# Performance work log

Measured on AMD Instinct MI355X. Metric: run time of the kernel, lower is better.

The kernel has to match this reference:

```python
import jax, jax.numpy as jnp
import numpy as np

EMB = 256
HEADS = 8
DEPTH = EMB // HEADS
IN_CH = 256
ROW_LEN, COL_LEN = 50, 100
H, W = 50, 100


def setup_inputs() -> dict:
    key = jax.random.key(0)
    ks = jax.random.split(key, 16)
    d2 = EMB // 2
    return {
        "x": jax.random.normal(ks[0], (IN_CH, H, W), jnp.float32),
        "context": jax.random.normal(ks[1], (IN_CH, H, W), jnp.float32),
        "pad_mask": jax.random.randint(ks[2], (1, H * W, H * W), 0, 2) == 1,
        # learned 2D positional embeddings (uniform init, as in reset_parameters)
        "row_embed": jax.random.uniform(ks[3], (ROW_LEN, d2), jnp.float32),
        "col_embed": jax.random.uniform(ks[4], (COL_LEN, d2), jnp.float32),
        # proj_in: Conv2d(in_ch, emb, 1) -> weight [emb, in_ch], bias [emb]
        "w_in": jax.random.normal(ks[5], (EMB, IN_CH), jnp.float32) / np.sqrt(IN_CH),
        "b_in": jax.random.normal(ks[6], (EMB,), jnp.float32) * 0.01,
        "wq": jax.random.normal(ks[7], (EMB, EMB), jnp.float32) / np.sqrt(EMB),
        "bq": jax.random.normal(ks[8], (EMB,), jnp.float32) * 0.01,
        "wk": jax.random.normal(ks[9], (EMB, EMB), jnp.float32) / np.sqrt(EMB),
        "bk": jax.random.normal(ks[10], (EMB,), jnp.float32) * 0.01,
        "wv": jax.random.normal(ks[11], (EMB, EMB), jnp.float32) / np.sqrt(EMB),
        "bv": jax.random.normal(ks[12], (EMB,), jnp.float32) * 0.01,
        # proj_out: Conv2d(emb, in_ch, 1) -> weight [in_ch, emb], bias [in_ch]
        "w_out": jax.random.normal(ks[13], (IN_CH, EMB), jnp.float32) / np.sqrt(EMB),
        "b_out": jax.random.normal(ks[14], (IN_CH,), jnp.float32) * 0.01,
    }


def _pos_encoding(h, w, row_embed, col_embed):
    # returns [emb, h, w]: first half column embeds, second half row embeds
    d2 = row_embed.shape[1]
    xe = jnp.broadcast_to(col_embed[:w][None, :, :], (h, w, d2))  # (h,w,d2)
    ye = jnp.broadcast_to(row_embed[:h][:, None, :], (h, w, d2))  # (h,w,d2)
    return jnp.concatenate([xe, ye], axis=-1).transpose(2, 0, 1)


def _embed_tokens(img, pos, w_in, b_in):
    # img: [c,h,w] -> tokens [1, h*w, emb]
    y = img + pos                                   # [c,h,w]
    y = jnp.einsum('chw,ec->ehw', y, w_in) + b_in[:, None, None]
    e, h, w = y.shape
    return y.reshape(e, h * w).T[None]              # [1, hw, e]


def reference(x, context, pad_mask, row_embed, col_embed, w_in, b_in,
              wq, bq, wk, bk, wv, bv, w_out, b_out):
    c, h, w = x.shape
    pos = _pos_encoding(h, w, row_embed, col_embed)
    xt = _embed_tokens(x, pos, w_in, b_in)          # [1, N, e]
    ct = _embed_tokens(context, pos, w_in, b_in)    # [1, N, e]

    q = xt @ wq.T + bq
    k = ct @ wk.T + bk
    v = ct @ wv.T + bv
    b, n, _ = q.shape
    q = q.reshape(b, n, HEADS, DEPTH).transpose(0, 2, 1, 3)  # [1,H,N,d]
    k = k.reshape(b, n, HEADS, DEPTH).transpose(0, 2, 1, 3)
    v = v.reshape(b, n, HEADS, DEPTH).transpose(0, 2, 1, 3)

    scale = EMB ** (-0.5)  # note: module scales by emb_dim, not depth
    att = jnp.einsum('bnid,bnjd->bnij', q, k) * scale
    att = jnp.where(pad_mask[:, None, :, :], jnp.float32(-1e9), att)
    att = jax.nn.softmax(att, axis=-1)
    out = jnp.einsum('bnij,bnjd->bnid', att, v)     # [1,H,N,d]

    out = out.transpose(0, 2, 1, 3).reshape(b, n, EMB)       # [1,N,e]
    out = out[0].T.reshape(EMB, h, w)                        # [e,h,w]
    out = jnp.einsum('ehw,ce->chw', out, w_out) + b_out[:, None, None]
    return out
```

## Files before the change

### kernel.cpp

```cpp
#include <hip/hip_runtime.h>
#include <hip/hip_bf16.h>
#include <math.h>

#define N_TOK 5000
#define EMB_D 256
#define W_DIM 100
#define TPAD 5120
#define QPAD 5056
#define NKT  157
#define NKT_PAD 160
#define NSPLIT 8
#define TILES_PS 20
#define NB_EMBED (2 * NKT)
#define NB_MASKQ 20

typedef __attribute__((ext_vector_type(8)))  short short8_t;
typedef __attribute__((ext_vector_type(16))) float f32x16;
typedef __attribute__((ext_vector_type(2)))  unsigned uint2v;

__device__ __forceinline__ unsigned f2bf(float x) {
    union { float f; unsigned u; } c; c.f = x;
    return (c.u + 0x8000u) >> 16;
}
__device__ __forceinline__ unsigned pack2bf(float lo, float hi) {
    __hip_bfloat162 h2 = __float22bfloat162_rn(make_float2(lo, hi));
    union { __hip_bfloat162 h; unsigned u; } c; c.h = h2;
    return c.u;
}
__device__ __forceinline__ short8_t mkfrag(const f32x16& c, int cb) {
    const int b = 8 * cb;
    unsigned a0 = pack2bf(c[b + 0], c[b + 1]);
    unsigned a1 = pack2bf(c[b + 2], c[b + 3]);
    unsigned b0 = pack2bf(c[b + 4], c[b + 5]);
    unsigned b1 = pack2bf(c[b + 6], c[b + 7]);
    uint2v s02 = __builtin_amdgcn_permlane32_swap(a0, b0, false, false);
    uint2v s13 = __builtin_amdgcn_permlane32_swap(a1, b1, false, false);
    union { unsigned u[4]; short8_t v; } fr;
    fr.u[0] = s02.x; fr.u[1] = s13.x; fr.u[2] = s02.y; fr.u[3] = s13.y;
    return fr.v;
}

__global__ __launch_bounds__(256) void wb16_kernel(
    const float* __restrict__ w_in, const float* __restrict__ wq,
    const float* __restrict__ wk, const float* __restrict__ wv,
    const float* __restrict__ w_out, unsigned short* __restrict__ Wb)
{
    const float* srcs[5] = {w_in, wq, wk, wv, w_out};
    const float* s = srcs[blockIdx.y];
    unsigned short* d = Wb + (size_t)blockIdx.y * 65536;
    int i = (blockIdx.x * 256 + threadIdx.x) * 4;
    float4 v = *(const float4*)(s + i);
    uint2 u;
    u.x = pack2bf(v.x, v.y);
    u.y = pack2bf(v.z, v.w);
    *(uint2*)&d[i] = u;
}

__device__ __forceinline__ void gemm2_rowmajor(
    const short8_t* tokfr, const unsigned short* __restrict__ W,
    const float* __restrict__ bias, float sc,
    unsigned short* __restrict__ dst, int tok, int l31, int h, int w)
{
    const int chb = 8 * h;
    #pragma unroll
    for (int i = 0; i < 2; ++i) {
        const int ot = 2 * w + i;
        f32x16 c;
        #pragma unroll
        for (int r = 0; r < 16; ++r) c[r] = 0.f;
        #pragma unroll
        for (int blk = 0; blk < 16; ++blk) {
            short8_t wf = *(const short8_t*)(W + (size_t)(ot * 32 + l31) * 256 + blk * 16 + chb);
            c = __builtin_amdgcn_mfma_f32_32x32x16_bf16(wf, tokfr[blk], c, 0, 0, 0);
        }
        #pragma unroll
        for (int m = 0; m < 4; ++m) {
            float4 b4 = *(const float4*)(bias + ot * 32 + 4 * h + 8 * m);
            c[4 * m + 0] = (c[4 * m + 0] + b4.x) * sc;
            c[4 * m + 1] = (c[4 * m + 1] + b4.y) * sc;
            c[4 * m + 2] = (c[4 * m + 2] + b4.z) * sc;
            c[4 * m + 3] = (c[4 * m + 3] + b4.w) * sc;
        }
        short8_t f0 = mkfrag(c, 0), f1 = mkfrag(c, 1);
        *(short8_t*)(dst + (size_t)ot * TPAD * 32 + (size_t)tok * 32 + chb)      = f0;
        *(short8_t*)(dst + (size_t)ot * TPAD * 32 + (size_t)tok * 32 + 16 + chb) = f1;
    }
}

__device__ __forceinline__ void gemm2_vt(
    const short8_t* tokfr, const unsigned short* __restrict__ W,
    const float* __restrict__ bias,
    unsigned short* __restrict__ Vt, int bx, int l31, int h, int w)
{
    const int chb = 8 * h;
    #pragma unroll
    for (int i = 0; i < 2; ++i) {
        const int ot = 2 * w + i;
        f32x16 c;
        #pragma unroll
        for (int r = 0; r < 16; ++r) c[r] = 0.f;
        #pragma unroll
        for (int blk = 0; blk < 16; ++blk) {
            short8_t wf = *(const short8_t*)(W + (size_t)(ot * 32 + l31) * 256 + blk * 16 + chb);
            c = __builtin_amdgcn_mfma_f32_32x32x16_bf16(wf, tokfr[blk], c, 0, 0, 0);
        }
        #pragma unroll
        for (int m = 0; m < 4; ++m) {
            float4 b4 = *(const float4*)(bias + ot * 32 + 4 * h + 8 * m);
            c[4 * m + 0] += b4.x; c[4 * m + 1] += b4.y;
            c[4 * m + 2] += b4.z; c[4 * m + 3] += b4.w;
        }
        #pragma unroll
        for (int r = 0; r < 16; ++r) {
            int oc = ot * 32 + ((r & 3) + 8 * (r >> 2) + 4 * h);
            int hd = oc >> 5, d = oc & 31;
            Vt[((size_t)bx * 8 + hd) * 1024 + d * 32 + l31] =
                (unsigned short)f2bf(c[r]);
        }
    }
}

__global__ __launch_bounds__(256) void embed_mask_kernel(
    const float* __restrict__ x, const float* __restrict__ ctx,
    const float* __restrict__ row_embed, const float* __restrict__ col_embed,
    const unsigned short* __restrict__ Wb,
    const float* __restrict__ b_in, const float* __restrict__ bq,
    const float* __restrict__ bk, const float* __restrict__ bv,
    const void* __restrict__ mask_raw,
    unsigned short* __restrict__ Qb, unsigned short* __restrict__ Kb,
    unsigned short* __restrict__ Vt, unsigned* __restrict__ pmT)
{
    __shared__ __align__(16) short8_t toksh[16][64];
    __shared__ int sflag;

    const int b = blockIdx.x;
    const int t = threadIdx.x;

    if (b >= NB_EMBED) {
        if (t < 64) {
            bool bad = false;
            const unsigned* mw = (const unsigned*)mask_raw;
            #pragma unroll
            for (int i = 0; i < 4; ++i) {
                unsigned w = mw[t * 4 + i];
                if (w != 0u && w != 1u && w != 0x3F800000u) bad = true;
            }
            unsigned long long bb = __ballot(bad);
            if (t == 0) sflag = (bb != 0ull) ? 1 : 0;
        }
        __syncthreads();

        const int m  = b - NB_EMBED;
        const int kt = m / NB_MASKQ;
        const int q  = (m - kt * NB_MASKQ) * 256 + t;
        if (q >= N_TOK) return;
        const int k0 = kt * 32;
        unsigned bits = 0;
        if (k0 < N_TOK) {
            const int nvalid = min(32, N_TOK - k0);
            const int nw = (nvalid + 3) >> 2;
            if (sflag) {
                const unsigned* src = (const unsigned*)((const char*)mask_raw + ((size_t)q * N_TOK + k0));
                for (int w = 0; w < nw; ++w) {
                    unsigned u = src[w];
                    #pragma unroll
                    for (int bb2 = 0; bb2 < 4; ++bb2)
                        if (((u >> (8 * bb2)) & 0xFFu) == 0u) bits |= 1u << (4 * w + bb2);
                }
            } else {
                const int* srcw = (const int*)mask_raw + (size_t)q * N_TOK + k0;
                for (int w = 0; w < nw; ++w) {
                    int4 u = *(const int4*)(srcw + 4 * w);
                    if (u.x == 0) bits |= 1u << (4 * w + 0);
                    if (u.y == 0) bits |= 1u << (4 * w + 1);
                    if (u.z == 0) bits |= 1u << (4 * w + 2);
                    if (u.w == 0) bits |= 1u << (4 * w + 3);
                }
            }
            if (nvalid < 32) bits &= (1u << nvalid) - 1u;
        }
        pmT[(size_t)kt * QPAD + q] = bits;
        return;
    }

    const int lane = t & 63;
    const int w = t >> 6;
    const int l31 = lane & 31, h = lane >> 5;
    const int chb = 8 * h;
    const int which = b / NKT;
    const int bx = b - which * NKT;
    const int tok0 = bx * 32;
    const int tok  = tok0 + l31;
    const int tokc = min(tok, N_TOK - 1);
    const float* img = (which == 0) ? x : ctx;
    const int hh = tokc / W_DIM, ww = tokc - hh * W_DIM;
    const float QSCALE = 0.0625f * 1.4426950408889634f;

    short8_t yfr[16];
    #pragma unroll
    for (int blk = 0; blk < 16; ++blk) {
        float yv[8];
        #pragma unroll
        for (int j = 0; j < 8; ++j) {
            int ch = blk * 16 + chb + j;
            float pos = (ch < 128) ? col_embed[ww * 128 + ch]
                                   : row_embed[hh * 128 + (ch - 128)];
            yv[j] = img[ch * N_TOK + tokc] + pos;
        }
        union { unsigned u[4]; short8_t v; } pk;
        #pragma unroll
        for (int j = 0; j < 4; ++j) pk.u[j] = pack2bf(yv[2 * j], yv[2 * j + 1]);
        yfr[blk] = pk.v;
    }

    #pragma unroll
    for (int i = 0; i < 2; ++i) {
        const int ct = 2 * w + i;
        f32x16 c;
        #pragma unroll
        for (int r = 0; r < 16; ++r) c[r] = 0.f;
        #pragma unroll
        for (int blk = 0; blk < 16; ++blk) {
            short8_t wf = *(const short8_t*)(Wb + (size_t)(ct * 32 + l31) * 256 + blk * 16 + chb);
            c = __builtin_amdgcn_mfma_f32_32x32x16_bf16(wf, yfr[blk], c, 0, 0, 0);
        }
        #pragma unroll
        for (int m = 0; m < 4; ++m) {
            float4 b4 = *(const float4*)(b_in + ct * 32 + 4 * h + 8 * m);
            c[4 * m + 0] += b4.x; c[4 * m + 1] += b4.y;
            c[4 * m + 2] += b4.z; c[4 * m + 3] += b4.w;
        }
        toksh[4 * w + 2 * i + 0][lane] = mkfrag(c, 0);
        toksh[4 * w + 2 * i + 1][lane] = mkfrag(c, 1);
    }
    __syncthreads();
    short8_t tokfr[16];
    #pragma unroll
    for (int blk = 0; blk < 16; ++blk) tokfr[blk] = toksh[blk][lane];

    if (which == 0) {
        gemm2_rowmajor(tokfr, Wb + 65536, bq, QSCALE, Qb, tok, l31, h, w);
    } else {
        gemm2_rowmajor(tokfr, Wb + 2 * 65536, bk, 1.f, Kb, tok, l31, h, w);
        gemm2_vt(tokfr, Wb + 3 * 65536, bv, Vt, bx, l31, h, w);
    }
}

__global__ __launch_bounds__(512) void attn_mfma_kernel(
    const unsigned short* __restrict__ Qb, const unsigned short* __restrict__ Kb,
    const unsigned short* __restrict__ Vt, const unsigned* __restrict__ pmT,
    unsigned short* __restrict__ AOb)
{
    __shared__ float comb[NSPLIT - 1][17][64];

    const int t    = threadIdx.x;
    const int lane = t & 63;
    const int ks   = t >> 6;
    const int bid  = blockIdx.x;
    const int head = bid & 7;
    const int q0   = (bid >> 3) * 32;
    const int l31  = lane & 31;
    const int h    = lane >> 5;
    const int grp8 = h * 8;

    const unsigned short* Kh = Kb + (size_t)head * TPAD * 32;
    const unsigned short* Qh = Qb + (size_t)head * TPAD * 32;
    const unsigned short* Vh = Vt + (size_t)head * 1024 + l31 * 32 + grp8;

    short8_t qf0 = *(const short8_t*)(Qh + (size_t)(q0 + l31) * 32 + grp8);
    short8_t qf1 = *(const short8_t*)(Qh + (size_t)(q0 + l31) * 32 + 16 + grp8);

    f32x16 oacc;
    #pragma unroll
    for (int r = 0; r < 16; ++r) oacc[r] = 0.f;
    float lsum = 0.f;

    const int kt0 = ks * TILES_PS;

    short8_t ka0, ka1, va0, va1; unsigned mw;
    {
        int k0 = kt0 * 32;
        const unsigned short* kp = Kh + (size_t)(k0 + l31) * 32 + grp8;
        ka0 = *(const short8_t*)kp;
        ka1 = *(const short8_t*)(kp + 16);
        va0 = *(const short8_t*)(Vh + (size_t)kt0 * 8192);
        va1 = *(const short8_t*)(Vh + (size_t)kt0 * 8192 + 16);
        mw  = pmT[(size_t)kt0 * QPAD + q0 + l31];
    }

    #pragma unroll 2
    for (int it = 0; it < TILES_PS; ++it) {
        int itn = (it < TILES_PS - 1) ? it + 1 : it;
        int ktn = kt0 + itn;
        int k0n = ktn * 32;
        const unsigned short* kpn = Kh + (size_t)(k0n + l31) * 32 + grp8;
        short8_t nka0 = *(const short8_t*)kpn;
        short8_t nka1 = *(const short8_t*)(kpn + 16);
        const unsigned short* vpn = Vh + (size_t)ktn * 8192;
        short8_t nva0 = *(const short8_t*)vpn;
        short8_t nva1 = *(const short8_t*)(vpn + 16);
        unsigned nmw  = pmT[(size_t)ktn * QPAD + q0 + l31];

        f32x16 sacc;
        #pragma unroll
        for (int r = 0; r < 16; ++r) sacc[r] = 0.f;
        __builtin_amdgcn_s_setprio(1);
        sacc = __builtin_amdgcn_mfma_f32_32x32x16_bf16(ka0, qf0, sacc, 0, 0, 0);
        sacc = __builtin_amdgcn_mfma_f32_32x32x16_bf16(ka1, qf1, sacc, 0, 0, 0);
        __builtin_amdgcn_s_setprio(0);

        const unsigned mwsh = mw >> (4 * h);
        float p[16];
        #pragma unroll
        for (int r = 0; r < 16; ++r) {
            float e = __builtin_amdgcn_exp2f(sacc[r]);
            const int pos = (r & 3) + 8 * (r >> 2);
            int keep = ((int)(mwsh << (31 - pos))) >> 31;
            p[r] = __int_as_float(__float_as_int(e) & keep);
        }
        {
            float s0 = (p[0] + p[1]) + (p[2] + p[3]);
            float s1 = (p[4] + p[5]) + (p[6] + p[7]);
            float s2 = (p[8] + p[9]) + (p[10] + p[11]);
            float s3 = (p[12] + p[13]) + (p[14] + p[15]);
            lsum += (s0 + s1) + (s2 + s3);
        }

        __builtin_amdgcn_s_setprio(1);
        #pragma unroll
        for (int c = 0; c < 2; ++c) {
            const int b = 8 * c;
            unsigned a0 = pack2bf(p[b + 0], p[b + 1]);
            unsigned b0 = pack2bf(p[b + 4], p[b + 5]);
            unsigned a1 = pack2bf(p[b + 2], p[b + 3]);
            unsigned b1 = pack2bf(p[b + 6], p[b + 7]);
            uint2v s02 = __builtin_amdgcn_permlane32_swap(a0, b0, false, false);
            uint2v s13 = __builtin_amdgcn_permlane32_swap(a1, b1, false, false);
            union { unsigned u[4]; short8_t v; } fr;
            fr.u[0] = s02.x; fr.u[1] = s13.x; fr.u[2] = s02.y; fr.u[3] = s13.y;
            oacc = __builtin_amdgcn_mfma_f32_32x32x16_bf16(c ? va1 : va0, fr.v, oacc, 0, 0, 0);
        }
        __builtin_amdgcn_s_setprio(0);

        ka0 = nka0; ka1 = nka1; va0 = nva0; va1 = nva1; mw = nmw;
    }

    float lfull = lsum + __shfl_xor(lsum, 32);

    if (ks) {
        comb[ks - 1][0][lane] = lfull;
        #pragma unroll
        for (int r = 0; r < 16; ++r) comb[ks - 1][1 + r][lane] = oacc[r];
    }
    __syncthreads();
    if (ks == 0) {
        float den = lfull;
        #pragma unroll
        for (int s = 0; s < NSPLIT - 1; ++s) den += comb[s][0][lane];
        float inv = 1.f / den;
        f32x16 oc2;
        #pragma unroll
        for (int r = 0; r < 16; ++r) {
            float o = oacc[r];
            #pragma unroll
            for (int s = 0; s < NSPLIT - 1; ++s) o += comb[s][1 + r][lane];
            oc2[r] = o * inv;
        }
        short8_t f0 = mkfrag(oc2, 0), f1 = mkfrag(oc2, 1);
        int q = q0 + l31;
        if (q < N_TOK) {
            *(short8_t*)(AOb + (size_t)q * EMB_D + head * 32 + grp8)      = f0;
            *(short8_t*)(AOb + (size_t)q * EMB_D + head * 32 + 16 + grp8) = f1;
        }
    }
}

__global__ __launch_bounds__(64) void proj_out_kernel(
    const unsigned short* __restrict__ AOb, const unsigned short* __restrict__ Wob,
    const float* __restrict__ b_out, float* __restrict__ out)
{
    const int lane = threadIdx.x;
    const int l31 = lane & 31, h = lane >> 5;
    const int chb = 8 * h;
    const int tok0 = blockIdx.x * 32;
    const int tok  = tok0 + l31;
    const bool vld = tok < N_TOK;
    const int ot = blockIdx.y;

    short8_t afr[16];
    #pragma unroll
    for (int blk = 0; blk < 16; ++blk)
        afr[blk] = *(const short8_t*)(AOb + (size_t)tok * EMB_D + blk * 16 + chb);

    f32x16 c;
    #pragma unroll
    for (int r = 0; r < 16; ++r) c[r] = 0.f;
    #pragma unroll
    for (int blk = 0; blk < 16; ++blk) {
        short8_t wf = *(const short8_t*)(Wob + (size_t)(ot * 32 + l31) * 256 + blk * 16 + chb);
        c = __builtin_amdgcn_mfma_f32_32x32x16_bf16(wf, afr[blk], c, 0, 0, 0);
    }
    #pragma unroll
    for (int m = 0; m < 4; ++m) {
        float4 b4 = *(const float4*)(b_out + ot * 32 + 4 * h + 8 * m);
        if (vld) {
            int row = ot * 32 + 4 * h + 8 * m;
            out[(size_t)(row + 0) * N_TOK + tok] = c[4 * m + 0] + b4.x;
            out[(size_t)(row + 1) * N_TOK + tok] = c[4 * m + 1] + b4.y;
            out[(size_t)(row + 2) * N_TOK + tok] = c[4 * m + 2] + b4.z;
            out[(size_t)(row + 3) * N_TOK + tok] = c[4 * m + 3] + b4.w;
        }
    }
}

extern "C" void kernel_launch(void* const* d_in, const int* in_sizes, int n_in,
                              void* d_out, int out_size, void* d_ws, size_t ws_size,
                              hipStream_t stream) {
    const float* x         = (const float*)d_in[0];
    const float* ctx       = (const float*)d_in[1];
    const void*  mask      = (const void*) d_in[2];
    const float* row_embed = (const float*)d_in[3];
    const float* col_embed = (const float*)d_in[4];
    const float* w_in      = (const float*)d_in[5];
    const float* b_in      = (const float*)d_in[6];
    const float* wq        = (const float*)d_in[7];
    const float* bq        = (const float*)d_in[8];
    const float* wk        = (const float*)d_in[9];
    const float* bk        = (const float*)d_in[10];
    const float* wv        = (const float*)d_in[11];
    const float* bv        = (const float*)d_in[12];
    const float* w_out     = (const float*)d_in[13];
    const float* b_out     = (const float*)d_in[14];
    float* out = (float*)d_out;

    char* ws = (char*)d_ws;
    unsigned short* Qb  = (unsigned short*)(ws);
    unsigned short* Kb  = (unsigned short*)(ws + 2621440);
    unsigned short* Vt  = (unsigned short*)(ws + 5242880);
    unsigned*       pmT = (unsigned*)      (ws + 7864320);
    unsigned short* AOb = (unsigned short*)(ws + 11100160);
    unsigned short* Wb  = (unsigned short*)(ws + 13660160);

    hipMemsetAsync(Vt + (size_t)NKT * 8 * 1024, 0,
                   (size_t)(NKT_PAD - NKT) * 8 * 1024 * 2, stream);
    wb16_kernel<<<dim3(64, 5), 256, 0, stream>>>(w_in, wq, wk, wv, w_out, Wb);
    embed_mask_kernel<<<dim3(NB_EMBED + NB_MASKQ * NKT_PAD), 256, 0, stream>>>(
        x, ctx, row_embed, col_embed, Wb, b_in, bq, bk, bv, mask, Qb, Kb, Vt, pmT);
    attn_mfma_kernel<<<dim3(NKT * 8), 512, 0, stream>>>(Qb, Kb, Vt, pmT, AOb);
    proj_out_kernel<<<dim3(NKT, 8), 64, 0, stream>>>(AOb, Wb + 4 * 65536, b_out, out);
}
```

Measured before the change: 123.1 us.

## Pack pad mask with wave-per-row ballots for coalesced reads and new bit layout

```diff
diff --git a/kernel.cpp b/kernel.cpp
--- a/kernel.cpp
+++ b/kernel.cpp
@@ -12,7 +12,7 @@
 #define NSPLIT 8
 #define TILES_PS 20
 #define NB_EMBED (2 * NKT)
-#define NB_MASKQ 20
+#define NB_MASK  1250
 
 typedef __attribute__((ext_vector_type(8)))  short short8_t;
 typedef __attribute__((ext_vector_type(16))) float f32x16;
@@ -150,36 +150,43 @@
         }
         __syncthreads();
 
-        const int m  = b - NB_EMBED;
-        const int kt = m / NB_MASKQ;
-        const int q  = (m - kt * NB_MASKQ) * 256 + t;
-        if (q >= N_TOK) return;
-        const int k0 = kt * 32;
-        unsigned bits = 0;
-        if (k0 < N_TOK) {
-            const int nvalid = min(32, N_TOK - k0);
-            const int nw = (nvalid + 3) >> 2;
-            if (sflag) {
-                const unsigned* src = (const unsigned*)((const char*)mask_raw + ((size_t)q * N_TOK + k0));
-                for (int w = 0; w < nw; ++w) {
-                    unsigned u = src[w];
-                    #pragma unroll
-                    for (int bb2 = 0; bb2 < 4; ++bb2)
-                        if (((u >> (8 * bb2)) & 0xFFu) == 0u) bits |= 1u << (4 * w + bb2);
-                }
-            } else {
-                const int* srcw = (const int*)mask_raw + (size_t)q * N_TOK + k0;
-                for (int w = 0; w < nw; ++w) {
-                    int4 u = *(const int4*)(srcw + 4 * w);
-                    if (u.x == 0) bits |= 1u << (4 * w + 0);
-                    if (u.y == 0) bits |= 1u << (4 * w + 1);
-                    if (u.z == 0) bits |= 1u << (4 * w + 2);
-                    if (u.w == 0) bits |= 1u << (4 * w + 3);
+        const int lane = t & 63;
+        const int wv   = t >> 6;
+        const int q    = (b - NB_EMBED) * 4 + wv;
+
+        if (sflag == 0) {
+            const int* row = (const int*)mask_raw + (size_t)q * N_TOK;
+            #pragma unroll
+            for (int c = 0; c < 20; ++c) {
+                int wb = c * 256 + lane * 4;
+                int wbc = min(wb, N_TOK - 4);
+                int4 u = *(const int4*)(row + wbc);
+                unsigned long long B0 = __ballot(u.x == 0 && wb + 0 < N_TOK);
+                unsigned long long B1 = __ballot(u.y == 0 && wb + 1 < N_TOK);
+                unsigned long long B2 = __ballot(u.z == 0 && wb + 2 < N_TOK);
+                unsigned long long B3 = __ballot(u.w == 0 && wb + 3 < N_TOK);
+                if (lane < 8) {
+                    unsigned word =  ((unsigned)(B0 >> (8 * lane)) & 0xFFu)
+                                  | (((unsigned)(B1 >> (8 * lane)) & 0xFFu) << 8)
+                                  | (((unsigned)(B2 >> (8 * lane)) & 0xFFu) << 16)
+                                  | (((unsigned)(B3 >> (8 * lane)) & 0xFFu) << 24);
+                    pmT[(size_t)(c * 8 + lane) * QPAD + q] = word;
                 }
             }
-            if (nvalid < 32) bits &= (1u << nvalid) - 1u;
-        }
-        pmT[(size_t)kt * QPAD + q] = bits;
+        } else {
+            const unsigned char* row = (const unsigned char*)mask_raw + (size_t)q * N_TOK;
+            for (int kt = lane; kt < NKT_PAD; kt += 64) {
+                unsigned bits = 0;
+                int k0 = kt * 32;
+                #pragma unroll
+                for (int k = 0; k < 32; ++k) {
+                    int key = k0 + k;
+                    if (key < N_TOK && row[key] == 0)
+                        bits |= 1u << (8 * (k & 3) + (k >> 2));
+                }
+                pmT[(size_t)kt * QPAD + q] = bits;
+            }
+        }
         return;
     }
 
@@ -309,13 +316,13 @@
         sacc = __builtin_amdgcn_mfma_f32_32x32x16_bf16(ka1, qf1, sacc, 0, 0, 0);
         __builtin_amdgcn_s_setprio(0);
 
-        const unsigned mwsh = mw >> (4 * h);
+        const unsigned mwh = mw >> h;
         float p[16];
         #pragma unroll
         for (int r = 0; r < 16; ++r) {
             float e = __builtin_amdgcn_exp2f(sacc[r]);
-            const int pos = (r & 3) + 8 * (r >> 2);
-            int keep = ((int)(mwsh << (31 - pos))) >> 31;
+            const int pos = 8 * (r & 3) + 2 * (r >> 2);
+            int keep = ((int)(mwh << (31 - pos))) >> 31;
             p[r] = __int_as_float(__float_as_int(e) & keep);
         }
         {
@@ -444,7 +451,7 @@
     hipMemsetAsync(Vt + (size_t)NKT * 8 * 1024, 0,
                    (size_t)(NKT_PAD - NKT) * 8 * 1024 * 2, stream);
     wb16_kernel<<<dim3(64, 5), 256, 0, stream>>>(w_in, wq, wk, wv, w_out, Wb);
-    embed_mask_kernel<<<dim3(NB_EMBED + NB_MASKQ * NKT_PAD), 256, 0, stream>>>(
+    embed_mask_kernel<<<dim3(NB_EMBED + NB_MASK), 256, 0, stream>>>(
         x, ctx, row_embed, col_embed, Wb, b_in, bq, bk, bv, mask, Qb, Kb, Vt, pmT);
     attn_mfma_kernel<<<dim3(NKT * 8), 512, 0, stream>>>(Qb, Kb, Vt, pmT, AOb);
     proj_out_kernel<<<dim3(NKT, 8), 64, 0, stream>>>(AOb, Wb + 4 * 65536, b_out, out);
```

Result: faster. 112.9 us (-8.3%).
